# Performance work log

Hardware: AMD Instinct MI355X
Metric: run time of the kernel (lower is better)

## Reference

```python
import jax, jax.numpy as jnp
import numpy as np

B, T, N, D = 8, 12, 512, 128
K = 16                      # number of pattern clusters
GEO_H, SEM_H, T_H = 4, 2, 2
HD = D // (GEO_H + SEM_H + T_H)      # 16
SCALE = HD ** -0.5
GD, SD, TD = GEO_H * HD, SEM_H * HD, T_H * HD  # 64, 32, 32


def setup_inputs() -> dict:
    key = jax.random.key(0)
    ks = jax.random.split(key, 24)
    w = lambda k, o, i: jax.random.normal(k, (o, i), jnp.float32) * 0.02
    return {
        'x': jax.random.normal(ks[0], (B, T, N, D), jnp.float32),
        'x_patterns': jax.random.normal(ks[1], (B, T, N, D, 1), jnp.float32),
        'pattern_keys': jax.random.normal(ks[2], (K, D, 1), jnp.float32),
        'dynamic_adj': jax.random.normal(ks[3], (B, N, N), jnp.float32) * 0.1,
        'geo_mask': jax.random.randint(ks[4], (N, N), 0, 2).astype(bool),
        'sem_mask': jax.random.randint(ks[5], (N, N), 0, 2).astype(bool),
        't_qw': w(ks[6], TD, D), 't_kw': w(ks[7], TD, D), 't_vw': w(ks[8], TD, D),
        'geo_qw': w(ks[9], GD, D), 'geo_kw': w(ks[10], GD, D), 'geo_vw': w(ks[11], GD, D),
        'sem_qw': w(ks[12], SD, D), 'sem_kw': w(ks[13], SD, D), 'sem_vw': w(ks[14], SD, D),
        'pat_qw': w(ks[15], GD, D), 'pat_qb': jax.random.normal(ks[16], (GD,), jnp.float32) * 0.02,
        'pat_kw': w(ks[17], GD, D), 'pat_kb': jax.random.normal(ks[18], (GD,), jnp.float32) * 0.02,
        'pat_vw': w(ks[19], GD, D), 'pat_vb': jax.random.normal(ks[20], (GD,), jnp.float32) * 0.02,
        'proj_w': w(ks[21], D, D), 'proj_b': jax.random.normal(ks[22], (D,), jnp.float32) * 0.02,
    }


def reference(x, x_patterns, pattern_keys, dynamic_adj, geo_mask, sem_mask,
              t_qw, t_kw, t_vw, geo_qw, geo_kw, geo_vw, sem_qw, sem_kw, sem_vw,
              pat_qw, pat_qb, pat_kw, pat_kb, pat_vw, pat_vb, proj_w, proj_b):
    Bc, Tc, Nc, Dc = x.shape
    proj3 = lambda z, w: jnp.einsum('btnd,ed->btne', z, w)  # 1x1 conv over channels

    # ---- temporal branch: attention over T per node ----
    def t_heads(z):  # (B,T,N,TD) -> (B,N,h,T,hd)
        return z.transpose(0, 2, 1, 3).reshape(Bc, Nc, Tc, T_H, HD).transpose(0, 1, 3, 2, 4)
    tq, tk, tv = t_heads(proj3(x, t_qw)), t_heads(proj3(x, t_kw)), t_heads(proj3(x, t_vw))
    t_attn = jax.nn.softmax(jnp.einsum('bnhqd,bnhkd->bnhqk', tq, tk) * SCALE, axis=-1)
    t_x = jnp.einsum('bnhqk,bnhkd->bnhqd', t_attn, tv)
    t_x = t_x.transpose(0, 1, 3, 2, 4).reshape(Bc, Nc, Tc, TD).transpose(0, 2, 1, 3)  # (B,T,N,TD)

    # ---- geo branch: pattern attention augments geo_k ----
    geo_q, geo_k, geo_v = proj3(x, geo_qw), proj3(x, geo_kw), proj3(x, geo_vw)
    pq = x_patterns[..., 0] @ pat_qw.T + pat_qb          # (B,T,N,GD)
    pk = pattern_keys[..., 0] @ pat_kw.T + pat_kb        # (K,GD)
    pv = pattern_keys[..., 0] @ pat_vw.T + pat_vb        # (K,GD)
    p_attn = jax.nn.softmax(jnp.einsum('btne,ke->btnk', pq, pk) * SCALE, axis=-1)
    geo_k = geo_k + jnp.einsum('btnk,ke->btne', p_attn, pv)

    def s_heads(z, h):  # (B,T,N,h*hd) -> (B,T,h,N,hd)
        return z.reshape(Bc, Tc, Nc, h, HD).transpose(0, 1, 3, 2, 4)
    gq, gk, gv = s_heads(geo_q, GEO_H), s_heads(geo_k, GEO_H), s_heads(geo_v, GEO_H)
    g_attn = jnp.einsum('bthqd,bthkd->bthqk', gq, gk) * SCALE
    g_attn = g_attn + dynamic_adj[:, None, None]         # dynamic bias
    g_attn = jnp.where(geo_mask, -jnp.inf, g_attn)
    g_attn = jax.nn.softmax(g_attn, axis=-1)
    geo_x = jnp.einsum('bthqk,bthkd->bthqd', g_attn, gv)
    geo_x = geo_x.transpose(0, 1, 3, 2, 4).reshape(Bc, Tc, Nc, GD)

    # ---- semantic branch ----
    sq = s_heads(proj3(x, sem_qw), SEM_H)
    sk = s_heads(proj3(x, sem_kw), SEM_H)
    sv = s_heads(proj3(x, sem_vw), SEM_H)
    s_attn = jnp.einsum('bthqd,bthkd->bthqk', sq, sk) * SCALE
    s_attn = jnp.where(sem_mask, -jnp.inf, s_attn)
    s_attn = jax.nn.softmax(s_attn, axis=-1)
    sem_x = jnp.einsum('bthqk,bthkd->bthqd', s_attn, sv)
    sem_x = sem_x.transpose(0, 1, 3, 2, 4).reshape(Bc, Tc, Nc, SD)

    out = jnp.concatenate([t_x, geo_x, sem_x], axis=-1) @ proj_w.T + proj_b
    return out
```

## Files before the change

kernel.cpp:

```cpp
#include <hip/hip_runtime.h>
#include <hip/hip_bf16.h>

using bf16 = __hip_bfloat16;
typedef __attribute__((ext_vector_type(8))) short short8;
typedef __attribute__((ext_vector_type(4))) float f32x4;

#define Bc 8
#define Tc 12
#define Nc 512
#define Dc 128
#define T_Hc 2
#define GEO_Hc 4
#define SEM_Hc 2
#define HDc 16
#define SCALEc 0.25f

constexpr size_t TSZ = (size_t)Bc * Nc * T_Hc * Tc * HDc;
constexpr size_t GSZ = (size_t)Bc * Tc * GEO_Hc * Nc * HDc;
constexpr size_t SSZ = (size_t)Bc * Tc * SEM_Hc * Nc * HDc;
constexpr size_t CSZ = (size_t)Bc * Tc * Nc * Dc;
constexpr size_t H_TQ = 0;
constexpr size_t H_TK = H_TQ + TSZ;
constexpr size_t H_TV = H_TK + TSZ;
constexpr size_t H_GQ = H_TV + TSZ;
constexpr size_t H_GK = H_GQ + GSZ;
constexpr size_t H_GV = H_GK + GSZ;
constexpr size_t H_SQ = H_GV + GSZ;
constexpr size_t H_SK = H_SQ + SSZ;
constexpr size_t H_SV = H_SK + SSZ;
constexpr size_t H_CC = H_SV + SSZ;
constexpr size_t H_END = H_CC + CSZ;
constexpr size_t F_PK = (H_END + 1) / 2;
constexpr size_t F_PV = F_PK + 1024;
constexpr size_t F_FLAG = F_PV + 1024;
constexpr size_t H_BG = H_TQ;
constexpr size_t H_BS = H_TQ + 2097152;

__device__ __forceinline__ float b2f(bf16 v) { return __bfloat162float(v); }
__device__ __forceinline__ bf16 f2b(float v) { return __float2bfloat16(v); }
__device__ __forceinline__ short f2bs(float v) {
    bf16 b = __float2bfloat16(v);
    return *reinterpret_cast<short*>(&b);
}
__device__ __forceinline__ float bs2f(short s) {
    union { unsigned u; float f; } x;
    x.u = ((unsigned)(unsigned short)s) << 16;
    return x.f;
}

__global__ __launch_bounds__(256) void k_prep(
    const float* __restrict__ pattern_keys, const float* __restrict__ pat_kw,
    const float* __restrict__ pat_kb, const float* __restrict__ pat_vw,
    const float* __restrict__ pat_vb, float* __restrict__ fws) {
    int idx = blockIdx.x * 256 + threadIdx.x;
    int which = idx >> 10;
    int r = idx & 1023;
    int k = r >> 6, e = r & 63;
    const float4* w = (const float4*)((which ? pat_vw : pat_kw) + (size_t)e * 128);
    const float4* pk = (const float4*)(pattern_keys + (size_t)k * 128);
    float acc = which ? pat_vb[e] : pat_kb[e];
#pragma unroll
    for (int j = 0; j < 32; ++j) {
        float4 a = pk[j], b = w[j];
        acc = fmaf(a.x, b.x, acc); acc = fmaf(a.y, b.y, acc);
        acc = fmaf(a.z, b.z, acc); acc = fmaf(a.w, b.w, acc);
    }
    fws[(which ? F_PV : F_PK) + (size_t)k * 64 + e] = acc;
}

__global__ __launch_bounds__(256) void k_maskdet(
    const unsigned char* __restrict__ mask, float* __restrict__ fws) {
    __shared__ int s_u8, s_odd4;
    int tid = threadIdx.x;
    if (tid == 0) { s_u8 = 0; s_odd4 = 0; }
    __syncthreads();
    int u8 = 0, odd4 = 0;
    for (int i = tid * 16; i < tid * 16 + 16; ++i) {
        unsigned char v = mask[i];
        if (v && (i & 3)) u8 = 1;
        if (v && ((i & 7) == 4)) odd4 = 1;
    }
    if (u8) atomicOr(&s_u8, 1);
    if (odd4) atomicOr(&s_odd4, 1);
    __syncthreads();
    if (tid == 0) fws[F_FLAG] = s_u8 ? 0.f : (s_odd4 ? 1.f : 2.f);
}

__global__ __launch_bounds__(256) void k_bias(
    const float* __restrict__ dyn, const unsigned char* __restrict__ gm,
    const unsigned char* __restrict__ sm, const float* __restrict__ fws,
    bf16* __restrict__ hb) {
    size_t gid = (size_t)blockIdx.x * 256 + threadIdx.x;
    int mode = (int)fws[F_FLAG];
    if (gid < 2097152) {
        size_t rem = gid & 262143;
        int mv = (mode == 0) ? (int)gm[rem]
               : (mode == 1) ? ((const int*)gm)[rem]
                             : ((const int*)gm)[2 * rem];
        hb[H_BG + gid] = f2b(mv ? -1e30f : dyn[gid]);
    } else if (gid < 2097152 + 262144) {
        size_t sid = gid - 2097152;
        int mv = (mode == 0) ? (int)sm[sid]
               : (mode == 1) ? ((const int*)sm)[sid]
                             : ((const int*)sm)[2 * sid];
        hb[H_BS + sid] = f2b(mv ? -1e30f : 0.f);
    }
}

__device__ __forceinline__ const float* wrow(
    int gc, const float* tq, const float* tk, const float* tv,
    const float* gq, const float* gk, const float* gv,
    const float* sq, const float* sk, const float* sv) {
    if (gc < 32) return tq + (size_t)gc * 128;
    if (gc < 64) return tk + (size_t)(gc - 32) * 128;
    if (gc < 96) return tv + (size_t)(gc - 64) * 128;
    if (gc < 160) return gq + (size_t)(gc - 96) * 128;
    if (gc < 224) return gk + (size_t)(gc - 160) * 128;
    if (gc < 288) return gv + (size_t)(gc - 224) * 128;
    if (gc < 320) return sq + (size_t)(gc - 288) * 128;
    if (gc < 352) return sk + (size_t)(gc - 320) * 128;
    return sv + (size_t)(gc - 352) * 128;
}

__global__ __launch_bounds__(256, 3) void k_projx(
    const float* __restrict__ x,
    const float* __restrict__ t_qw, const float* __restrict__ t_kw,
    const float* __restrict__ t_vw, const float* __restrict__ geo_qw,
    const float* __restrict__ geo_kw, const float* __restrict__ geo_vw,
    const float* __restrict__ sem_qw, const float* __restrict__ sem_kw,
    const float* __restrict__ sem_vw, bf16* __restrict__ hb) {
    __shared__ float xs[64 * 132];
    __shared__ float wsh[64 * 68];

    int tid = threadIdx.x;
    int tok0 = blockIdx.x * 64;
    int ty = tid >> 4, tx = tid & 15;

    for (int u = tid; u < 2048; u += 256) {
        int row = u >> 5, f4 = u & 31;
        *(float4*)&xs[row * 132 + f4 * 4] =
            *(const float4*)(x + (size_t)(tok0 + row) * 128 + f4 * 4);
    }

    for (int chunk = 0; chunk < 6; ++chunk) {
        float acc[4][4] = {};
        for (int kh = 0; kh < 2; ++kh) {
            __syncthreads();
            for (int u = tid; u < 1024; u += 256) {
                int row = u >> 4, f4 = u & 15;
                const float* src = wrow(chunk * 64 + row, t_qw, t_kw, t_vw,
                                        geo_qw, geo_kw, geo_vw, sem_qw, sem_kw,
                                        sem_vw) + kh * 64 + f4 * 4;
                *(float4*)&wsh[row * 68 + f4 * 4] = *(const float4*)src;
            }
            __syncthreads();
#pragma unroll 4
            for (int kk = 0; kk < 64; kk += 4) {
                float4 a[4], b[4];
#pragma unroll
                for (int i = 0; i < 4; ++i)
                    a[i] = *(const float4*)&xs[(ty + 16 * i) * 132 + kh * 64 + kk];
#pragma unroll
                for (int j = 0; j < 4; ++j)
                    b[j] = *(const float4*)&wsh[(tx + 16 * j) * 68 + kk];
#pragma unroll
                for (int i = 0; i < 4; ++i)
#pragma unroll
                    for (int j = 0; j < 4; ++j) {
                        acc[i][j] = fmaf(a[i].x, b[j].x, acc[i][j]);
                        acc[i][j] = fmaf(a[i].y, b[j].y, acc[i][j]);
                        acc[i][j] = fmaf(a[i].z, b[j].z, acc[i][j]);
                        acc[i][j] = fmaf(a[i].w, b[j].w, acc[i][j]);
                    }
            }
        }
#pragma unroll
        for (int i = 0; i < 4; ++i) {
            int token = tok0 + ty + 16 * i;
            int b = token / (Tc * Nc);
            int rr = token - b * Tc * Nc;
            int t = rr >> 9;
            int n = rr & 511;
#pragma unroll
            for (int j = 0; j < 4; ++j) {
                int gc = chunk * 64 + tx + 16 * j;
                float v = acc[i][j];
                size_t idx;
                if (gc < 96) {
                    int which = gc >> 5, hh = (gc >> 4) & 1, d = gc & 15;
                    size_t base = which == 0 ? H_TQ : which == 1 ? H_TK : H_TV;
                    idx = base + ((size_t)(b * Nc + n) * T_Hc + hh) * (Tc * HDc)
                          + t * HDc + d;
                } else if (gc < 288) {
                    int r2 = gc - 96;
                    int which = r2 >> 6, h = (r2 >> 4) & 3, d = gc & 15;
                    if (which == 0) v *= SCALEc;
                    size_t base = which == 0 ? H_GQ : which == 1 ? H_GK : H_GV;
                    idx = base + (((size_t)b * Tc + t) * GEO_Hc + h) * (Nc * HDc)
                          + n * HDc + d;
                } else {
                    int r2 = gc - 288;
                    int which = r2 >> 5, h = (r2 >> 4) & 1, d = gc & 15;
                    if (which == 0) v *= SCALEc;
                    size_t base = which == 0 ? H_SQ : which == 1 ? H_SK : H_SV;
                    idx = base + (((size_t)b * Tc + t) * SEM_Hc + h) * (Nc * HDc)
                          + n * HDc + d;
                }
                hb[idx] = f2b(v);
            }
        }
    }
}

__global__ __launch_bounds__(256, 2) void k_projp(
    const float* __restrict__ xp, const float* __restrict__ pat_qw,
    const float* __restrict__ pat_qb, const float* __restrict__ fws,
    bf16* __restrict__ hb) {
    __shared__ float xs[64 * 132];
    __shared__ float wsh[64 * 68];
    __shared__ float pks[1024], pvs[1024], pqbs[64];

    int tid = threadIdx.x;
    int tok0 = blockIdx.x * 64;
    int ty = tid >> 4, tx = tid & 15;

    for (int u = tid; u < 2048; u += 256) {
        int row = u >> 5, f4 = u & 31;
        *(float4*)&xs[row * 132 + f4 * 4] =
            *(const float4*)(xp + (size_t)(tok0 + row) * 128 + f4 * 4);
    }
    for (int u = tid; u < 1024; u += 256) {
        pks[u] = fws[F_PK + u];
        pvs[u] = fws[F_PV + u];
    }
    if (tid < 64) pqbs[tid] = pat_qb[tid];

    float acc[4][4] = {};
    for (int kh = 0; kh < 2; ++kh) {
        __syncthreads();
        for (int u = tid; u < 1024; u += 256) {
            int row = u >> 4, f4 = u & 15;
            *(float4*)&wsh[row * 68 + f4 * 4] =
                *(const float4*)(pat_qw + (size_t)row * 128 + kh * 64 + f4 * 4);
        }
        __syncthreads();
#pragma unroll 4
        for (int kk = 0; kk < 64; kk += 4) {
            float4 a[4], b[4];
#pragma unroll
            for (int i = 0; i < 4; ++i)
                a[i] = *(const float4*)&xs[(ty + 16 * i) * 132 + kh * 64 + kk];
#pragma unroll
            for (int j = 0; j < 4; ++j)
                b[j] = *(const float4*)&wsh[(tx + 16 * j) * 68 + kk];
#pragma unroll
            for (int i = 0; i < 4; ++i)
#pragma unroll
                for (int j = 0; j < 4; ++j) {
                    acc[i][j] = fmaf(a[i].x, b[j].x, acc[i][j]);
                    acc[i][j] = fmaf(a[i].y, b[j].y, acc[i][j]);
                    acc[i][j] = fmaf(a[i].z, b[j].z, acc[i][j]);
                    acc[i][j] = fmaf(a[i].w, b[j].w, acc[i][j]);
                }
        }
    }
    __syncthreads();
    float* pqs = xs;
    float* plogs = wsh;
#pragma unroll
    for (int i = 0; i < 4; ++i)
#pragma unroll
        for (int j = 0; j < 4; ++j)
            pqs[(ty + 16 * i) * 68 + tx + 16 * j] = acc[i][j] + pqbs[tx + 16 * j];
    __syncthreads();
    {
        int tok = tid >> 2, k4 = (tid & 3) * 4;
        for (int k = k4; k < k4 + 4; ++k) {
            float s = 0.f;
#pragma unroll 16
            for (int e = 0; e < 64; ++e)
                s = fmaf(pqs[tok * 68 + e], pks[k * 64 + e], s);
            plogs[tok * 17 + k] = s * SCALEc;
        }
    }
    __syncthreads();
    {
        int tok = tid >> 2, q = tid & 3;
        float mx = -1e30f;
        for (int k = 0; k < 16; ++k) mx = fmaxf(mx, plogs[tok * 17 + k]);
        float p[16], sum = 0.f;
        for (int k = 0; k < 16; ++k) {
            p[k] = __expf(plogs[tok * 17 + k] - mx);
            sum += p[k];
        }
        float inv = 1.f / sum;
        int token = tok0 + tok;
        int b = token / (Tc * Nc);
        int rr = token - b * Tc * Nc;
        int t = rr >> 9;
        int n = rr & 511;
        for (int cc = 0; cc < 16; ++cc) {
            int c = q * 16 + cc;
            float v = 0.f;
            for (int k = 0; k < 16; ++k) v = fmaf(p[k], pvs[k * 64 + c], v);
            v *= inv;
            size_t idx = H_GK + (((size_t)b * Tc + t) * GEO_Hc + (c >> 4)) * (Nc * HDc)
                         + n * HDc + (c & 15);
            hb[idx] = f2b(b2f(hb[idx]) + v);
        }
    }
}

__global__ __launch_bounds__(64) void k_tattn(bf16* __restrict__ hb) {
    int blk = blockIdx.x;
    int h = blk & 1;
    int bn = blk >> 1;
    int b = bn >> 9;
    int n = bn & 511;
    size_t base = ((size_t)(b * Nc + n) * T_Hc + h) * (Tc * HDc);

    __shared__ float q[192], kk[192], v[192], s[144];
    int tid = threadIdx.x;
    for (int u = tid; u < 192; u += 64) {
        q[u] = b2f(hb[H_TQ + base + u]);
        kk[u] = b2f(hb[H_TK + base + u]);
        v[u] = b2f(hb[H_TV + base + u]);
    }
    __syncthreads();
    for (int idx = tid; idx < 144; idx += 64) {
        int qi = idx / 12, ki = idx - qi * 12;
        float acc = 0.f;
#pragma unroll
        for (int d = 0; d < 16; ++d) acc = fmaf(q[qi * 16 + d], kk[ki * 16 + d], acc);
        s[idx] = acc * SCALEc;
    }
    __syncthreads();
    if (tid < 12) {
        float mx = -1e30f;
        for (int ki = 0; ki < 12; ++ki) mx = fmaxf(mx, s[tid * 12 + ki]);
        float sum = 0.f;
        for (int ki = 0; ki < 12; ++ki) {
            float p = __expf(s[tid * 12 + ki] - mx);
            s[tid * 12 + ki] = p;
            sum += p;
        }
        float inv = 1.f / sum;
        for (int ki = 0; ki < 12; ++ki) s[tid * 12 + ki] *= inv;
    }
    __syncthreads();
    for (int idx = tid; idx < 192; idx += 64) {
        int qi = idx >> 4, d = idx & 15;
        float acc = 0.f;
#pragma unroll
        for (int ki = 0; ki < 12; ++ki) acc = fmaf(s[qi * 12 + ki], v[ki * 16 + d], acc);
        hb[H_CC + (((size_t)b * Tc + qi) * Nc + n) * Dc + h * HDc + d] = f2b(acc);
    }
}

__global__ __launch_bounds__(256, 4) void k_attn2(
    bf16* __restrict__ hb, size_t QO, size_t KO, size_t VO, int H,
    const bf16* __restrict__ biasp, size_t bstride, int coff) {
    __shared__ short vt[16 * 512];
    __shared__ short pbuf[4][16 * 128];
    __shared__ float lt[4][16];
    __shared__ float at[4][16];

    int bid = blockIdx.x;
    int part = bid & 3;
    int bth_lin = bid >> 2;
    int h = bth_lin % H;
    int rest = bth_lin / H;
    int t = rest % Tc;
    int b = rest / Tc;

    size_t bth = (((size_t)b * Tc + t) * H + h) * (size_t)(Nc * HDc);
    const bf16* Qp = hb + QO + bth;
    const bf16* Kp = hb + KO + bth;
    const bf16* Vp = hb + VO + bth;
    const bf16* bp = biasp + (size_t)b * bstride;

    int tid = threadIdx.x;
    int w = tid >> 6;
    int lane = tid & 63;
    int l15 = lane & 15;
    int quad = lane >> 4;

    for (int idx = tid; idx < 8192; idx += 256) {
        int k = idx >> 4, d = idx & 15;
        int kk = ((((k >> 3) & 7) ^ (d & 7)) << 3) | (k & ~63) | (k & 7);
        vt[d * 512 + kk] = *reinterpret_cast<const short*>(Vp + idx);
    }
    __syncthreads();

    short* pw = &pbuf[w][0];
    float* lw = lt[w];
    float* aw = at[w];
    int sw = l15 & 7;

    for (int qq = 0; qq < 2; ++qq) {
        int q0 = part * 128 + w * 32 + qq * 16;
        int qg = q0 + l15;
        short8 bq = {0, 0, 0, 0, 0, 0, 0, 0};
        if (quad < 2) bq = *(const short8*)(Qp + (size_t)qg * 16 + quad * 8);

        float m_i = -3e38f, l_i = 0.f;
        f32x4 O = {0.f, 0.f, 0.f, 0.f};

        for (int ch = 0; ch < 4; ++ch) {
            int kabs0 = ch * 128;
            f32x4 S[8];
#pragma unroll
            for (int kt = 0; kt < 8; ++kt) {
                int kabs = kabs0 + kt * 16;
                short4 bb = *(const short4*)(bp + (size_t)qg * 512 + kabs + quad * 4);
                f32x4 c;
                c[0] = bs2f(bb.x); c[1] = bs2f(bb.y);
                c[2] = bs2f(bb.z); c[3] = bs2f(bb.w);
                short8 ak = {0, 0, 0, 0, 0, 0, 0, 0};
                if (quad < 2)
                    ak = *(const short8*)(Kp + (size_t)(kabs + l15) * 16 + quad * 8);
                S[kt] = __builtin_amdgcn_mfma_f32_16x16x32_bf16(ak, bq, c, 0, 0, 0);
            }
            float cm = S[0][0];
#pragma unroll
            for (int kt = 0; kt < 8; ++kt)
#pragma unroll
                for (int r = 0; r < 4; ++r) cm = fmaxf(cm, S[kt][r]);
            cm = fmaxf(cm, __shfl_xor(cm, 16));
            cm = fmaxf(cm, __shfl_xor(cm, 32));
            float mnew = fmaxf(m_i, cm);
            float alpha = __expf(m_i - mnew);
            m_i = mnew;
            float psum = 0.f;
#pragma unroll
            for (int kt = 0; kt < 8; ++kt) {
#pragma unroll
                for (int r = 0; r < 4; ++r) {
                    float p = __expf(S[kt][r] - mnew);
                    S[kt][r] = p;
                    psum += p;
                }
            }
            psum += __shfl_xor(psum, 16);
            psum += __shfl_xor(psum, 32);
            l_i = l_i * alpha + psum;
            if (quad == 0) aw[l15] = alpha;
#pragma unroll
            for (int kt = 0; kt < 8; ++kt) {
                short4 pk4;
                pk4.x = f2bs(S[kt][0]); pk4.y = f2bs(S[kt][1]);
                pk4.z = f2bs(S[kt][2]); pk4.w = f2bs(S[kt][3]);
                int g = 2 * kt + (quad >> 1);
                *(short4*)&pw[l15 * 128 + ((g ^ sw) << 3) + ((quad & 1) << 2)] = pk4;
            }
            float4 a4 = *(float4*)&aw[quad * 4];
            O[0] *= a4.x; O[1] *= a4.y; O[2] *= a4.z; O[3] *= a4.w;
#pragma unroll
            for (int kw = 0; kw < 4; ++kw) {
                int g = 4 * kw + quad;
                short8 ap = *(const short8*)&pw[l15 * 128 + ((g ^ sw) << 3)];
                short8 bv = *(const short8*)&vt[l15 * 512 + kabs0 + ((g ^ sw) << 3)];
                O = __builtin_amdgcn_mfma_f32_16x16x32_bf16(ap, bv, O, 0, 0, 0);
            }
        }
        if (quad == 0) lw[l15] = l_i;
        float4 l4 = *(float4*)&lw[quad * 4];
        float inv0 = 1.f / l4.x, inv1 = 1.f / l4.y, inv2 = 1.f / l4.z, inv3 = 1.f / l4.w;
        size_t obase = H_CC + (((size_t)b * Tc + t) * Nc + q0) * Dc + coff + h * HDc + l15;
        hb[obase + (size_t)(quad * 4 + 0) * Dc] = f2b(O[0] * inv0);
        hb[obase + (size_t)(quad * 4 + 1) * Dc] = f2b(O[1] * inv1);
        hb[obase + (size_t)(quad * 4 + 2) * Dc] = f2b(O[2] * inv2);
        hb[obase + (size_t)(quad * 4 + 3) * Dc] = f2b(O[3] * inv3);
    }
}

__global__ __launch_bounds__(256, 3) void k_out(
    const bf16* __restrict__ hb, const float* __restrict__ proj_w,
    const float* __restrict__ proj_b, float* __restrict__ out) {
    __shared__ float xs[64 * 132];
    __shared__ float wsh[64 * 68];
    __shared__ float pbs[128];

    int tid = threadIdx.x;
    int tok0 = blockIdx.x * 64;
    int ty = tid >> 4, tx = tid & 15;

    for (int u = tid; u < 1024; u += 256) {
        int row = u >> 4, seg = u & 15;
        uint4 raw = *(const uint4*)(hb + H_CC + (size_t)(tok0 + row) * 128 + seg * 8);
        float f[8];
        unsigned ua[4] = {raw.x, raw.y, raw.z, raw.w};
#pragma unroll
        for (int q = 0; q < 4; ++q) {
            union { unsigned u; float f; } lo, hi;
            lo.u = (ua[q] & 0xFFFFu) << 16;
            hi.u = ua[q] & 0xFFFF0000u;
            f[2 * q] = lo.f;
            f[2 * q + 1] = hi.f;
        }
        int base = row * 132 + seg * 8;
#pragma unroll
        for (int e = 0; e < 8; ++e) xs[base + e] = f[e];
    }
    if (tid < 128) pbs[tid] = proj_b[tid];

    for (int chunk = 0; chunk < 2; ++chunk) {
        float acc[4][4] = {};
        for (int kh = 0; kh < 2; ++kh) {
            __syncthreads();
            for (int u = tid; u < 1024; u += 256) {
                int row = u >> 4, f4 = u & 15;
                *(float4*)&wsh[row * 68 + f4 * 4] =
                    *(const float4*)(proj_w + (size_t)(chunk * 64 + row) * 128
                                     + kh * 64 + f4 * 4);
            }
            __syncthreads();
#pragma unroll 4
            for (int kk = 0; kk < 64; kk += 4) {
                float4 a[4], b[4];
#pragma unroll
                for (int i = 0; i < 4; ++i)
                    a[i] = *(const float4*)&xs[(ty + 16 * i) * 132 + kh * 64 + kk];
#pragma unroll
                for (int j = 0; j < 4; ++j)
                    b[j] = *(const float4*)&wsh[(tx + 16 * j) * 68 + kk];
#pragma unroll
                for (int i = 0; i < 4; ++i)
#pragma unroll
                    for (int j = 0; j < 4; ++j) {
                        acc[i][j] = fmaf(a[i].x, b[j].x, acc[i][j]);
                        acc[i][j] = fmaf(a[i].y, b[j].y, acc[i][j]);
                        acc[i][j] = fmaf(a[i].z, b[j].z, acc[i][j]);
                        acc[i][j] = fmaf(a[i].w, b[j].w, acc[i][j]);
                    }
            }
        }
#pragma unroll
        for (int i = 0; i < 4; ++i) {
            int token = tok0 + ty + 16 * i;
#pragma unroll
            for (int j = 0; j < 4; ++j) {
                int ch = chunk * 64 + tx + 16 * j;
                out[(size_t)token * 128 + ch] = acc[i][j] + pbs[ch];
            }
        }
    }
}

extern "C" void kernel_launch(void* const* d_in, const int* in_sizes, int n_in,
                              void* d_out, int out_size, void* d_ws, size_t ws_size,
                              hipStream_t stream) {
    const float* x = (const float*)d_in[0];
    const float* xp = (const float*)d_in[1];
    const float* pattern_keys = (const float*)d_in[2];
    const float* dyn = (const float*)d_in[3];
    const void* geo_mask = d_in[4];
    const void* sem_mask = d_in[5];
    const float* t_qw = (const float*)d_in[6];
    const float* t_kw = (const float*)d_in[7];
    const float* t_vw = (const float*)d_in[8];
    const float* geo_qw = (const float*)d_in[9];
    const float* geo_kw = (const float*)d_in[10];
    const float* geo_vw = (const float*)d_in[11];
    const float* sem_qw = (const float*)d_in[12];
    const float* sem_kw = (const float*)d_in[13];
    const float* sem_vw = (const float*)d_in[14];
    const float* pat_qw = (const float*)d_in[15];
    const float* pat_qb = (const float*)d_in[16];
    const float* pat_kw = (const float*)d_in[17];
    const float* pat_kb = (const float*)d_in[18];
    const float* pat_vw = (const float*)d_in[19];
    const float* pat_vb = (const float*)d_in[20];
    const float* proj_w = (const float*)d_in[21];
    const float* proj_b = (const float*)d_in[22];

    bf16* hb = (bf16*)d_ws;
    float* fws = (float*)d_ws;

    k_prep<<<8, 256, 0, stream>>>(pattern_keys, pat_kw, pat_kb, pat_vw, pat_vb, fws);
    k_maskdet<<<1, 256, 0, stream>>>((const unsigned char*)geo_mask, fws);
    k_projx<<<768, 256, 0, stream>>>(x, t_qw, t_kw, t_vw, geo_qw, geo_kw, geo_vw,
                                     sem_qw, sem_kw, sem_vw, hb);
    k_projp<<<768, 256, 0, stream>>>(xp, pat_qw, pat_qb, fws, hb);
    k_tattn<<<Bc * Nc * T_Hc, 64, 0, stream>>>(hb);
    k_bias<<<9216, 256, 0, stream>>>(dyn, (const unsigned char*)geo_mask,
                                     (const unsigned char*)sem_mask, fws, hb);
    k_attn2<<<Bc * Tc * GEO_Hc * 4, 256, 0, stream>>>(
        hb, H_GQ, H_GK, H_GV, GEO_Hc, hb + H_BG, (size_t)Nc * Nc, 32);
    k_attn2<<<Bc * Tc * SEM_Hc * 4, 256, 0, stream>>>(
        hb, H_SQ, H_SK, H_SV, SEM_Hc, hb + H_BS, 0, 96);
    k_out<<<768, 256, 0, stream>>>(hb, proj_w, proj_b, (float*)d_out);
}
```

Measured before the change: 412.9 us.

## Move input and output projections to bf16 MFMA with split-precision activations

The FP32 FMA GEMMs for the fused QKV input projection and the output projection are replaced with MFMA 16x16x32 bf16 kernels. A new kernel converts the weights to bf16 in the workspace up front, duplicating each input-projection weight so that x, split into hi and lo bf16 parts, keeps near-fp32 accuracy. The output projection uses plain bf16 on the already-bf16 concat buffer. Shared-memory tiles use an XOR swizzle, and each block now covers 128 tokens, giving half as many blocks, at the cost of one extra small launch.

```diff
diff --git a/kernel.cpp b/kernel.cpp
--- a/kernel.cpp
+++ b/kernel.cpp
@@ -33,6 +33,8 @@
 constexpr size_t F_PK = (H_END + 1) / 2;
 constexpr size_t F_PV = F_PK + 1024;
 constexpr size_t F_FLAG = F_PV + 1024;
+constexpr size_t H_W2X = 2 * (F_FLAG + 64);
+constexpr size_t H_W2O = H_W2X + 384 * 256;
 constexpr size_t H_BG = H_TQ;
 constexpr size_t H_BS = H_TQ + 2097152;
 
@@ -84,6 +86,44 @@
     if (odd4) atomicOr(&s_odd4, 1);
     __syncthreads();
     if (tid == 0) fws[F_FLAG] = s_u8 ? 0.f : (s_odd4 ? 1.f : 2.f);
+}
+
+__device__ __forceinline__ const float* wrow(
+    int gc, const float* tq, const float* tk, const float* tv,
+    const float* gq, const float* gk, const float* gv,
+    const float* sq, const float* sk, const float* sv) {
+    if (gc < 32) return tq + (size_t)gc * 128;
+    if (gc < 64) return tk + (size_t)(gc - 32) * 128;
+    if (gc < 96) return tv + (size_t)(gc - 64) * 128;
+    if (gc < 160) return gq + (size_t)(gc - 96) * 128;
+    if (gc < 224) return gk + (size_t)(gc - 160) * 128;
+    if (gc < 288) return gv + (size_t)(gc - 224) * 128;
+    if (gc < 320) return sq + (size_t)(gc - 288) * 128;
+    if (gc < 352) return sk + (size_t)(gc - 320) * 128;
+    return sv + (size_t)(gc - 352) * 128;
+}
+
+__global__ __launch_bounds__(256) void k_wcvt(
+    const float* __restrict__ t_qw, const float* __restrict__ t_kw,
+    const float* __restrict__ t_vw, const float* __restrict__ geo_qw,
+    const float* __restrict__ geo_kw, const float* __restrict__ geo_vw,
+    const float* __restrict__ sem_qw, const float* __restrict__ sem_kw,
+    const float* __restrict__ sem_vw, const float* __restrict__ proj_w,
+    bf16* __restrict__ hb) {
+    int gid = blockIdx.x * 256 + threadIdx.x;
+    if (gid < 49152) {
+        int row = gid >> 7, k = gid & 127;
+        const float* src = wrow(row, t_qw, t_kw, t_vw, geo_qw, geo_kw, geo_vw,
+                                sem_qw, sem_kw, sem_vw);
+        float v = src[k];
+        if ((row >= 96 && row < 160) || (row >= 288 && row < 320)) v *= SCALEc;
+        bf16 bv = f2b(v);
+        hb[H_W2X + (size_t)row * 256 + 2 * k] = bv;
+        hb[H_W2X + (size_t)row * 256 + 2 * k + 1] = bv;
+    } else {
+        int g = gid - 49152;
+        hb[H_W2O + g] = f2b(proj_w[g]);
+    }
 }
 
 __global__ __launch_bounds__(256) void k_bias(
@@ -107,106 +147,89 @@
     }
 }
 
-__device__ __forceinline__ const float* wrow(
-    int gc, const float* tq, const float* tk, const float* tv,
-    const float* gq, const float* gk, const float* gv,
-    const float* sq, const float* sk, const float* sv) {
-    if (gc < 32) return tq + (size_t)gc * 128;
-    if (gc < 64) return tk + (size_t)(gc - 32) * 128;
-    if (gc < 96) return tv + (size_t)(gc - 64) * 128;
-    if (gc < 160) return gq + (size_t)(gc - 96) * 128;
-    if (gc < 224) return gk + (size_t)(gc - 160) * 128;
-    if (gc < 288) return gv + (size_t)(gc - 224) * 128;
-    if (gc < 320) return sq + (size_t)(gc - 288) * 128;
-    if (gc < 352) return sk + (size_t)(gc - 320) * 128;
-    return sv + (size_t)(gc - 352) * 128;
-}
-
-__global__ __launch_bounds__(256, 3) void k_projx(
-    const float* __restrict__ x,
-    const float* __restrict__ t_qw, const float* __restrict__ t_kw,
-    const float* __restrict__ t_vw, const float* __restrict__ geo_qw,
-    const float* __restrict__ geo_kw, const float* __restrict__ geo_vw,
-    const float* __restrict__ sem_qw, const float* __restrict__ sem_kw,
-    const float* __restrict__ sem_vw, bf16* __restrict__ hb) {
-    __shared__ float xs[64 * 132];
-    __shared__ float wsh[64 * 68];
+__global__ __launch_bounds__(256, 2) void k_projx(
+    const float* __restrict__ x, bf16* __restrict__ hb) {
+    __shared__ short xs[128 * 256];
 
     int tid = threadIdx.x;
-    int tok0 = blockIdx.x * 64;
-    int ty = tid >> 4, tx = tid & 15;
-
-    for (int u = tid; u < 2048; u += 256) {
-        int row = u >> 5, f4 = u & 31;
-        *(float4*)&xs[row * 132 + f4 * 4] =
-            *(const float4*)(x + (size_t)(tok0 + row) * 128 + f4 * 4);
-    }
-
-    for (int chunk = 0; chunk < 6; ++chunk) {
-        float acc[4][4] = {};
-        for (int kh = 0; kh < 2; ++kh) {
-            __syncthreads();
-            for (int u = tid; u < 1024; u += 256) {
-                int row = u >> 4, f4 = u & 15;
-                const float* src = wrow(chunk * 64 + row, t_qw, t_kw, t_vw,
-                                        geo_qw, geo_kw, geo_vw, sem_qw, sem_kw,
-                                        sem_vw) + kh * 64 + f4 * 4;
-                *(float4*)&wsh[row * 68 + f4 * 4] = *(const float4*)src;
+    int m0 = blockIdx.x * 128;
+    int b = m0 / (Tc * Nc);
+    int rr = m0 - b * Tc * Nc;
+    int t = rr >> 9;
+    int n0 = rr & 511;
+
+    for (int u = tid; u < 4096; u += 256) {
+        int row = u >> 5, g = u & 31;
+        float4 v = *(const float4*)(x + (size_t)(m0 + row) * 128 + g * 4);
+        short8 s;
+        short h0 = f2bs(v.x); s[0] = h0; s[1] = f2bs(v.x - bs2f(h0));
+        short h1 = f2bs(v.y); s[2] = h1; s[3] = f2bs(v.y - bs2f(h1));
+        short h2 = f2bs(v.z); s[4] = h2; s[5] = f2bs(v.z - bs2f(h2));
+        short h3 = f2bs(v.w); s[6] = h3; s[7] = f2bs(v.w - bs2f(h3));
+        *(short8*)&xs[row * 256 + ((g ^ (row & 7)) << 3)] = s;
+    }
+    __syncthreads();
+
+    int w = tid >> 6;
+    int lane = tid & 63;
+    int l15 = lane & 15;
+    int quad = lane >> 4;
+    const bf16* w2 = hb + H_W2X;
+
+    for (int nc = 0; nc < 6; ++nc) {
+        f32x4 acc[2][4];
+#pragma unroll
+        for (int i = 0; i < 2; ++i)
+#pragma unroll
+            for (int j = 0; j < 4; ++j) acc[i][j] = (f32x4){0.f, 0.f, 0.f, 0.f};
+
+#pragma unroll
+        for (int ks = 0; ks < 8; ++ks) {
+            int r0 = w * 32 + l15;
+            int r1 = r0 + 16;
+            short8 a0 = *(const short8*)&xs[r0 * 256 + (((ks * 4 + quad) ^ (r0 & 7)) << 3)];
+            short8 a1 = *(const short8*)&xs[r1 * 256 + (((ks * 4 + quad) ^ (r1 & 7)) << 3)];
+#pragma unroll
+            for (int nj = 0; nj < 4; ++nj) {
+                short8 bfr = *(const short8*)(w2 + (size_t)(nc * 64 + nj * 16 + l15) * 256
+                                              + ks * 32 + quad * 8);
+                acc[0][nj] = __builtin_amdgcn_mfma_f32_16x16x32_bf16(a0, bfr, acc[0][nj], 0, 0, 0);
+                acc[1][nj] = __builtin_amdgcn_mfma_f32_16x16x32_bf16(a1, bfr, acc[1][nj], 0, 0, 0);
             }
-            __syncthreads();
-#pragma unroll 4
-            for (int kk = 0; kk < 64; kk += 4) {
-                float4 a[4], b[4];
-#pragma unroll
-                for (int i = 0; i < 4; ++i)
-                    a[i] = *(const float4*)&xs[(ty + 16 * i) * 132 + kh * 64 + kk];
-#pragma unroll
-                for (int j = 0; j < 4; ++j)
-                    b[j] = *(const float4*)&wsh[(tx + 16 * j) * 68 + kk];
-#pragma unroll
-                for (int i = 0; i < 4; ++i)
-#pragma unroll
-                    for (int j = 0; j < 4; ++j) {
-                        acc[i][j] = fmaf(a[i].x, b[j].x, acc[i][j]);
-                        acc[i][j] = fmaf(a[i].y, b[j].y, acc[i][j]);
-                        acc[i][j] = fmaf(a[i].z, b[j].z, acc[i][j]);
-                        acc[i][j] = fmaf(a[i].w, b[j].w, acc[i][j]);
+        }
+#pragma unroll
+        for (int nj = 0; nj < 4; ++nj) {
+            int gc = nc * 64 + nj * 16 + l15;
+            int tile16 = nc * 4 + nj;
+            int d = gc & 15;
+#pragma unroll
+            for (int i = 0; i < 2; ++i) {
+                int nrow0 = n0 + w * 32 + i * 16 + quad * 4;
+#pragma unroll
+                for (int r = 0; r < 4; ++r) {
+                    int n = nrow0 + r;
+                    float v = acc[i][nj][r];
+                    size_t idx;
+                    if (tile16 < 6) {
+                        int which = gc >> 5, hh = (gc >> 4) & 1;
+                        size_t base = which == 0 ? H_TQ : which == 1 ? H_TK : H_TV;
+                        idx = base + ((size_t)(b * Nc + n) * T_Hc + hh) * (Tc * HDc)
+                              + t * HDc + d;
+                    } else if (tile16 < 18) {
+                        int r2 = gc - 96;
+                        int which = r2 >> 6, h = (r2 >> 4) & 3;
+                        size_t base = which == 0 ? H_GQ : which == 1 ? H_GK : H_GV;
+                        idx = base + (((size_t)b * Tc + t) * GEO_Hc + h) * (Nc * HDc)
+                              + n * HDc + d;
+                    } else {
+                        int r2 = gc - 288;
+                        int which = r2 >> 5, h = (r2 >> 4) & 1;
+                        size_t base = which == 0 ? H_SQ : which == 1 ? H_SK : H_SV;
+                        idx = base + (((size_t)b * Tc + t) * SEM_Hc + h) * (Nc * HDc)
+                              + n * HDc + d;
                     }
-            }
-        }
-#pragma unroll
-        for (int i = 0; i < 4; ++i) {
-            int token = tok0 + ty + 16 * i;
-            int b = token / (Tc * Nc);
-            int rr = token - b * Tc * Nc;
-            int t = rr >> 9;
-            int n = rr & 511;
-#pragma unroll
-            for (int j = 0; j < 4; ++j) {
-                int gc = chunk * 64 + tx + 16 * j;
-                float v = acc[i][j];
-                size_t idx;
-                if (gc < 96) {
-                    int which = gc >> 5, hh = (gc >> 4) & 1, d = gc & 15;
-                    size_t base = which == 0 ? H_TQ : which == 1 ? H_TK : H_TV;
-                    idx = base + ((size_t)(b * Nc + n) * T_Hc + hh) * (Tc * HDc)
-                          + t * HDc + d;
-                } else if (gc < 288) {
-                    int r2 = gc - 96;
-                    int which = r2 >> 6, h = (r2 >> 4) & 3, d = gc & 15;
-                    if (which == 0) v *= SCALEc;
-                    size_t base = which == 0 ? H_GQ : which == 1 ? H_GK : H_GV;
-                    idx = base + (((size_t)b * Tc + t) * GEO_Hc + h) * (Nc * HDc)
-                          + n * HDc + d;
-                } else {
-                    int r2 = gc - 288;
-                    int which = r2 >> 5, h = (r2 >> 4) & 1, d = gc & 15;
-                    if (which == 0) v *= SCALEc;
-                    size_t base = which == 0 ? H_SQ : which == 1 ? H_SK : H_SV;
-                    idx = base + (((size_t)b * Tc + t) * SEM_Hc + h) * (Nc * HDc)
-                          + n * HDc + d;
+                    hb[idx] = f2b(v);
                 }
-                hb[idx] = f2b(v);
             }
         }
     }
@@ -474,74 +497,59 @@
     }
 }
 
-__global__ __launch_bounds__(256, 3) void k_out(
-    const bf16* __restrict__ hb, const float* __restrict__ proj_w,
-    const float* __restrict__ proj_b, float* __restrict__ out) {
-    __shared__ float xs[64 * 132];
-    __shared__ float wsh[64 * 68];
+__global__ __launch_bounds__(256, 3) void k_outm(
+    const bf16* __restrict__ hb, const float* __restrict__ proj_b,
+    float* __restrict__ out) {
+    __shared__ short cs[128 * 128];
     __shared__ float pbs[128];
 
     int tid = threadIdx.x;
-    int tok0 = blockIdx.x * 64;
-    int ty = tid >> 4, tx = tid & 15;
-
-    for (int u = tid; u < 1024; u += 256) {
-        int row = u >> 4, seg = u & 15;
-        uint4 raw = *(const uint4*)(hb + H_CC + (size_t)(tok0 + row) * 128 + seg * 8);
-        float f[8];
-        unsigned ua[4] = {raw.x, raw.y, raw.z, raw.w};
-#pragma unroll
-        for (int q = 0; q < 4; ++q) {
-            union { unsigned u; float f; } lo, hi;
-            lo.u = (ua[q] & 0xFFFFu) << 16;
-            hi.u = ua[q] & 0xFFFF0000u;
-            f[2 * q] = lo.f;
-            f[2 * q + 1] = hi.f;
-        }
-        int base = row * 132 + seg * 8;
-#pragma unroll
-        for (int e = 0; e < 8; ++e) xs[base + e] = f[e];
+    int m0 = blockIdx.x * 128;
+
+    for (int u = tid; u < 2048; u += 256) {
+        int row = u >> 4, g = u & 15;
+        *(short8*)&cs[row * 128 + ((g ^ (row & 7)) << 3)] =
+            *(const short8*)(hb + H_CC + (size_t)(m0 + row) * 128 + g * 8);
     }
     if (tid < 128) pbs[tid] = proj_b[tid];
-
-    for (int chunk = 0; chunk < 2; ++chunk) {
-        float acc[4][4] = {};
-        for (int kh = 0; kh < 2; ++kh) {
-            __syncthreads();
-            for (int u = tid; u < 1024; u += 256) {
-                int row = u >> 4, f4 = u & 15;
-                *(float4*)&wsh[row * 68 + f4 * 4] =
-                    *(const float4*)(proj_w + (size_t)(chunk * 64 + row) * 128
-                                     + kh * 64 + f4 * 4);
-            }
-            __syncthreads();
-#pragma unroll 4
-            for (int kk = 0; kk < 64; kk += 4) {
-                float4 a[4], b[4];
-#pragma unroll
-                for (int i = 0; i < 4; ++i)
-                    a[i] = *(const float4*)&xs[(ty + 16 * i) * 132 + kh * 64 + kk];
-#pragma unroll
-                for (int j = 0; j < 4; ++j)
-                    b[j] = *(const float4*)&wsh[(tx + 16 * j) * 68 + kk];
-#pragma unroll
-                for (int i = 0; i < 4; ++i)
-#pragma unroll
-                    for (int j = 0; j < 4; ++j) {
-                        acc[i][j] = fmaf(a[i].x, b[j].x, acc[i][j]);
-                        acc[i][j] = fmaf(a[i].y, b[j].y, acc[i][j]);
-                        acc[i][j] = fmaf(a[i].z, b[j].z, acc[i][j]);
-                        acc[i][j] = fmaf(a[i].w, b[j].w, acc[i][j]);
-                    }
-            }
-        }
-#pragma unroll
-        for (int i = 0; i < 4; ++i) {
-            int token = tok0 + ty + 16 * i;
-#pragma unroll
-            for (int j = 0; j < 4; ++j) {
-                int ch = chunk * 64 + tx + 16 * j;
-                out[(size_t)token * 128 + ch] = acc[i][j] + pbs[ch];
+    __syncthreads();
+
+    int w = tid >> 6;
+    int lane = tid & 63;
+    int l15 = lane & 15;
+    int quad = lane >> 4;
+    const bf16* w2o = hb + H_W2O;
+
+    f32x4 acc[2][8];
+#pragma unroll
+    for (int i = 0; i < 2; ++i)
+#pragma unroll
+        for (int j = 0; j < 8; ++j) acc[i][j] = (f32x4){0.f, 0.f, 0.f, 0.f};
+
+#pragma unroll
+    for (int ks = 0; ks < 4; ++ks) {
+        int r0 = w * 32 + l15;
+        int r1 = r0 + 16;
+        short8 a0 = *(const short8*)&cs[r0 * 128 + (((ks * 4 + quad) ^ (r0 & 7)) << 3)];
+        short8 a1 = *(const short8*)&cs[r1 * 128 + (((ks * 4 + quad) ^ (r1 & 7)) << 3)];
+#pragma unroll
+        for (int nj = 0; nj < 8; ++nj) {
+            short8 bfr = *(const short8*)(w2o + (size_t)(nj * 16 + l15) * 128
+                                          + ks * 32 + quad * 8);
+            acc[0][nj] = __builtin_amdgcn_mfma_f32_16x16x32_bf16(a0, bfr, acc[0][nj], 0, 0, 0);
+            acc[1][nj] = __builtin_amdgcn_mfma_f32_16x16x32_bf16(a1, bfr, acc[1][nj], 0, 0, 0);
+        }
+    }
+#pragma unroll
+    for (int i = 0; i < 2; ++i) {
+#pragma unroll
+        for (int nj = 0; nj < 8; ++nj) {
+            int ch = nj * 16 + l15;
+            float bias = pbs[ch];
+#pragma unroll
+            for (int r = 0; r < 4; ++r) {
+                int token = m0 + w * 32 + i * 16 + quad * 4 + r;
+                out[(size_t)token * 128 + ch] = acc[i][nj][r] + bias;
             }
         }
     }
@@ -579,8 +587,9 @@
 
     k_prep<<<8, 256, 0, stream>>>(pattern_keys, pat_kw, pat_kb, pat_vw, pat_vb, fws);
     k_maskdet<<<1, 256, 0, stream>>>((const unsigned char*)geo_mask, fws);
-    k_projx<<<768, 256, 0, stream>>>(x, t_qw, t_kw, t_vw, geo_qw, geo_kw, geo_vw,
-                                     sem_qw, sem_kw, sem_vw, hb);
+    k_wcvt<<<256, 256, 0, stream>>>(t_qw, t_kw, t_vw, geo_qw, geo_kw, geo_vw,
+                                    sem_qw, sem_kw, sem_vw, proj_w, hb);
+    k_projx<<<384, 256, 0, stream>>>(x, hb);
     k_projp<<<768, 256, 0, stream>>>(xp, pat_qw, pat_qb, fws, hb);
     k_tattn<<<Bc * Nc * T_Hc, 64, 0, stream>>>(hb);
     k_bias<<<9216, 256, 0, stream>>>(dyn, (const unsigned char*)geo_mask,
@@ -589,5 +598,5 @@
         hb, H_GQ, H_GK, H_GV, GEO_Hc, hb + H_BG, (size_t)Nc * Nc, 32);
     k_attn2<<<Bc * Tc * SEM_Hc * 4, 256, 0, stream>>>(
         hb, H_SQ, H_SK, H_SV, SEM_Hc, hb + H_BS, 0, 96);
-    k_out<<<768, 256, 0, stream>>>(hb, proj_w, proj_b, (float*)d_out);
-}
+    k_outm<<<384, 256, 0, stream>>>(hb, proj_b, (float*)d_out);
+}
```

New measurement: 364.7 us. 1.13x faster.
